# Performance work log

Measured on AMD Instinct MI355X. Metric: run time of the kernel, lower is better.

## Reference

```python
import jax, jax.numpy as jnp
import numpy as np

D_MODEL = 1024
NUM_HEADS = 16
D_K = D_MODEL // NUM_HEADS
B, T = 2, 2048


def setup_inputs() -> dict:
    key = jax.random.key(0)
    ks = jax.random.split(key, 9)
    s = 1.0 / np.sqrt(D_MODEL)
    inp = {"x": jax.random.normal(ks[0], (B, T, D_MODEL), dtype=jnp.float32)}
    for i, name in enumerate(["q", "k", "v", "out"]):
        inp[f"W_{name}"] = jax.random.uniform(ks[1 + 2 * i], (D_MODEL, D_MODEL), jnp.float32, -s, s)
        inp[f"b_{name}"] = jax.random.uniform(ks[2 + 2 * i], (D_MODEL,), jnp.float32, -s, s)
    return inp


def reference(x, W_q, b_q, W_k, b_k, W_v, b_v, W_out, b_out):
    b, t, _ = x.shape
    # torch Linear: y = x @ W.T + b
    def proj(inp, W, bias):
        y = inp @ W.T + bias
        return y.reshape(b, -1, NUM_HEADS, D_K).transpose(0, 2, 1, 3)  # [B,H,T,d_k]

    Q = proj(x, W_q, b_q)
    K = proj(x, W_k, b_k)
    V = proj(x, W_v, b_v)
    scores = jnp.einsum("bhqd,bhkd->bhqk", Q, K) / jnp.sqrt(jnp.float32(D_K))
    attn = jax.nn.softmax(scores, axis=-1)
    ctx = jnp.einsum("bhqk,bhkd->bhqd", attn, V)
    ctx = ctx.transpose(0, 2, 1, 3).reshape(b, t, D_MODEL)
    return ctx @ W_out.T + b_out
```

## Files before the change

### kernel.cpp

```cpp
#include <hip/hip_runtime.h>
#include <hip/hip_bf16.h>

typedef __attribute__((ext_vector_type(8))) short short8;
typedef __attribute__((ext_vector_type(4))) short short4v;
typedef __attribute__((ext_vector_type(4))) float floatx4;

__device__ __forceinline__ unsigned short f2b(float f) {
  unsigned int v;
  __builtin_memcpy(&v, &f, 4);
  unsigned int r = (v + 0x7FFFu + ((v >> 16) & 1u)) >> 16;
  return (unsigned short)r;
}

__device__ __forceinline__ unsigned int f2b_pk(float a, float b) {
  unsigned int ua, ub;
  __builtin_memcpy(&ua, &a, 4);
  __builtin_memcpy(&ub, &b, 4);
  ua = ua + 0x7FFFu + ((ua >> 16) & 1u);
  ub = ub + 0x7FFFu + ((ub >> 16) & 1u);
#if __has_builtin(__builtin_amdgcn_perm)
  return __builtin_amdgcn_perm(ub, ua, 0x07060302u);
#else
  return (ub & 0xFFFF0000u) | (ua >> 16);
#endif
}

__device__ __forceinline__ float fast_exp2(float x) {
#if __has_builtin(__builtin_amdgcn_exp2f)
  return __builtin_amdgcn_exp2f(x);
#else
  return __builtin_exp2f(x);
#endif
}

__device__ __forceinline__ void async_copy16(const void* g, void* l) {
  __builtin_amdgcn_global_load_lds(
      (const __attribute__((address_space(1))) unsigned int*)g,
      (__attribute__((address_space(3))) unsigned int*)l, 16, 0, 0);
}

#define QSCALE 0.18033688011112042f

__global__ __launch_bounds__(256) void cvt_all_kernel(
    const float* __restrict__ x,
    const float* __restrict__ w0, const float* __restrict__ w1,
    const float* __restrict__ w2, const float* __restrict__ w3,
    unsigned short* __restrict__ xb,
    unsigned short* __restrict__ d0, unsigned short* __restrict__ d1,
    unsigned short* __restrict__ d2, unsigned short* __restrict__ d3)
{
  int gid = blockIdx.x * 256 + threadIdx.x;
  const float* src;
  unsigned short* dst;
  size_t off;
  if (gid < (1 << 20)) {
    src = x; dst = xb; off = gid;
  } else {
    int g = gid - (1 << 20);
    int w = g >> 18;
    off = g & 0x3FFFF;
    src = (w == 0) ? w0 : (w == 1) ? w1 : (w == 2) ? w2 : w3;
    dst = (w == 0) ? d0 : (w == 1) ? d1 : (w == 2) ? d2 : d3;
  }
  floatx4 v = *(const floatx4*)(src + off * 4);
  unsigned int lo = f2b_pk(v[0], v[1]), hi = f2b_pk(v[2], v[3]);
  unsigned long long r = ((unsigned long long)hi << 32) | lo;
  *(unsigned long long*)(dst + off * 4) = r;
}

__global__ __launch_bounds__(256) void gemm_qkv_kernel(
    const unsigned short* __restrict__ A,
    const unsigned short* __restrict__ W0, const unsigned short* __restrict__ W1,
    const unsigned short* __restrict__ W2,
    const float* __restrict__ bias0, const float* __restrict__ bias1,
    const float* __restrict__ bias2,
    unsigned short* __restrict__ Qo, unsigned short* __restrict__ Ko,
    unsigned short* __restrict__ VTo)
{
  const int z = blockIdx.z;
  const unsigned short* W  = (z == 0) ? W0 : (z == 1) ? W1 : W2;
  const float* bias        = (z == 0) ? bias0 : (z == 1) ? bias1 : bias2;

  __shared__ alignas(16) unsigned short sA[128 * 32];
  __shared__ alignas(16) unsigned short sB[128 * 32];

  const int tid  = threadIdx.x;
  const int lane = tid & 63;
  const int wave = tid >> 6;
  const int col  = lane & 15;
  const int quad = lane >> 4;
  const int wm   = (wave >> 1) * 64;
  const int wn   = (wave & 1) * 64;
  const int m0   = blockIdx.y * 128;
  const int n0   = blockIdx.x * 128;
  const int swz8 = (quad ^ ((col >> 1) & 3)) * 8;

  floatx4 acc[4][4];
#pragma unroll
  for (int i = 0; i < 4; ++i)
#pragma unroll
    for (int j = 0; j < 4; ++j) acc[i][j] = (floatx4){0.f, 0.f, 0.f, 0.f};

  for (int k0 = 0; k0 < 1024; k0 += 32) {
    __syncthreads();
#pragma unroll
    for (int i = 0; i < 2; ++i) {
      int c   = i * 256 + tid;
      int row = c >> 2;
      int cs  = (c & 3) ^ ((c >> 3) & 3);
      int ko  = cs * 8;
      async_copy16(A + (size_t)(m0 + row) * 1024 + k0 + ko, sA + c * 8);
      async_copy16(W + (size_t)(n0 + row) * 1024 + k0 + ko, sB + c * 8);
    }
    __syncthreads();
    short8 af[4], bf[4];
#pragma unroll
    for (int mi = 0; mi < 4; ++mi)
      af[mi] = *(const short8*)(sA + (wm + mi * 16 + col) * 32 + swz8);
#pragma unroll
    for (int ni = 0; ni < 4; ++ni)
      bf[ni] = *(const short8*)(sB + (wn + ni * 16 + col) * 32 + swz8);
#pragma unroll
    for (int mi = 0; mi < 4; ++mi)
#pragma unroll
      for (int ni = 0; ni < 4; ++ni)
        acc[mi][ni] = __builtin_amdgcn_mfma_f32_16x16x32_bf16(af[mi], bf[ni], acc[mi][ni], 0, 0, 0);
  }

#pragma unroll
  for (int ni = 0; ni < 4; ++ni) {
    int n = n0 + wn + ni * 16 + col;
    float bv = bias[n];
#pragma unroll
    for (int mi = 0; mi < 4; ++mi) {
      int mbase = m0 + wm + mi * 16 + quad * 4;
      if (z == 2) {
        int d = n & 63, h = n >> 6;
        int bb = mbase >> 11, t = mbase & 2047;
        unsigned int lo = f2b_pk(acc[mi][ni][0] + bv, acc[mi][ni][1] + bv);
        unsigned int hi = f2b_pk(acc[mi][ni][2] + bv, acc[mi][ni][3] + bv);
        unsigned long long wv = ((unsigned long long)hi << 32) | lo;
        *(unsigned long long*)(VTo + (((size_t)bb * 16 + h) * 64 + d) * 2048 + t) = wv;
      } else {
#pragma unroll
        for (int r = 0; r < 4; ++r) {
          int m = mbase + r;
          float val = acc[mi][ni][r] + bv;
          if (z == 0) Qo[(size_t)m * 1024 + n] = f2b(val * QSCALE);
          else        Ko[(size_t)m * 1024 + n] = f2b(val);
        }
      }
    }
  }
}

__global__ __launch_bounds__(256) void gemm_out_kernel(
    const unsigned short* __restrict__ A, const unsigned short* __restrict__ W,
    const float* __restrict__ bias, float* __restrict__ DF)
{
  __shared__ alignas(16) unsigned short sA[128 * 32];
  __shared__ alignas(16) unsigned short sB[64 * 32];

  const int tid  = threadIdx.x;
  const int lane = tid & 63;
  const int wave = tid >> 6;
  const int col  = lane & 15;
  const int quad = lane >> 4;
  const int wm   = (wave >> 1) * 64;
  const int wn   = (wave & 1) * 32;
  const int m0   = blockIdx.y * 128;
  const int n0   = blockIdx.x * 64;
  const int swz8 = (quad ^ ((col >> 1) & 3)) * 8;

  floatx4 acc[4][2];
#pragma unroll
  for (int i = 0; i < 4; ++i)
#pragma unroll
    for (int j = 0; j < 2; ++j) acc[i][j] = (floatx4){0.f, 0.f, 0.f, 0.f};

  for (int k0 = 0; k0 < 1024; k0 += 32) {
    __syncthreads();
#pragma unroll
    for (int i = 0; i < 2; ++i) {
      int c   = i * 256 + tid;
      int row = c >> 2;
      int cs  = (c & 3) ^ ((c >> 3) & 3);
      async_copy16(A + (size_t)(m0 + row) * 1024 + k0 + cs * 8, sA + c * 8);
    }
    {
      int row = tid >> 2;
      int cs  = (tid & 3) ^ ((tid >> 3) & 3);
      async_copy16(W + (size_t)(n0 + row) * 1024 + k0 + cs * 8, sB + tid * 8);
    }
    __syncthreads();
    short8 af[4], bf[2];
#pragma unroll
    for (int mi = 0; mi < 4; ++mi)
      af[mi] = *(const short8*)(sA + (wm + mi * 16 + col) * 32 + swz8);
#pragma unroll
    for (int ni = 0; ni < 2; ++ni)
      bf[ni] = *(const short8*)(sB + (wn + ni * 16 + col) * 32 + swz8);
#pragma unroll
    for (int mi = 0; mi < 4; ++mi)
#pragma unroll
      for (int ni = 0; ni < 2; ++ni)
        acc[mi][ni] = __builtin_amdgcn_mfma_f32_16x16x32_bf16(af[mi], bf[ni], acc[mi][ni], 0, 0, 0);
  }

#pragma unroll
  for (int ni = 0; ni < 2; ++ni) {
    int n = n0 + wn + ni * 16 + col;
    float bv = bias[n];
#pragma unroll
    for (int mi = 0; mi < 4; ++mi) {
      int mbase = m0 + wm + mi * 16 + quad * 4;
#pragma unroll
      for (int r = 0; r < 4; ++r)
        DF[(size_t)(mbase + r) * 1024 + n] = acc[mi][ni][r] + bv;
    }
  }
}

__global__ __launch_bounds__(256, 2) void attention_kernel(
    const unsigned short* __restrict__ Q, const unsigned short* __restrict__ K,
    const unsigned short* __restrict__ VT, unsigned short* __restrict__ CTX)
{
  __shared__ alignas(16) unsigned short sK[2][4096];
  __shared__ alignas(16) unsigned short sV[2][4096];
  __shared__ alignas(16) unsigned short sP[4][32 * 64];

  const int flat = blockIdx.x;
  const int idx  = flat >> 3;
  const int bh   = (flat & 7) * 4 + (idx >> 4);
  const int q0   = (idx & 15) * 128;
  const int b = bh >> 4, h = bh & 15;

  const int tid  = threadIdx.x;
  const int lane = tid & 63;
  const int wave = tid >> 6;
  const int col  = lane & 15;
  const int quad = lane >> 4;
  const int c7   = col & 7;
  const int swz8 = (quad ^ ((col >> 1) & 3)) * 8;

  const int srow = tid >> 2;
  const int sko  = ((tid & 3) ^ ((tid >> 3) & 3)) * 8;

  const unsigned short* kbase = K + ((size_t)b * 2048 + srow) * 1024 + h * 64;
  const unsigned short* vbase = VT + ((size_t)bh * 64 + srow) * 2048;

  short8 qfA[2], qfB[2];
  {
    const unsigned short* qp =
        Q + ((size_t)(b * 2048 + q0 + wave * 32 + col)) * 1024 + h * 64 + quad * 8;
    qfA[0] = *(const short8*)qp;
    qfA[1] = *(const short8*)(qp + 32);
    qfB[0] = *(const short8*)(qp + 16 * 1024);
    qfB[1] = *(const short8*)(qp + 16 * 1024 + 32);
  }

#pragma unroll
  for (int i = 0; i < 2; ++i) {
    async_copy16(kbase + i * 32 + sko, sK[0] + (i * 256 + tid) * 8);
    async_copy16(vbase + i * 32 + sko, sV[0] + (i * 256 + tid) * 8);
  }

  floatx4 OA[4], OB[4];
#pragma unroll
  for (int f = 0; f < 4; ++f) {
    OA[f] = (floatx4){0.f, 0.f, 0.f, 0.f};
    OB[f] = (floatx4){0.f, 0.f, 0.f, 0.f};
  }
  float laccA = 0.f, laccB = 0.f;

  unsigned short* myP = &sP[wave][0];

#pragma unroll 2
  for (int kt = 0; kt < 2048; kt += 64) {
    const int cur = (kt >> 6) & 1;
    const unsigned short* sKc = sK[cur];
    const unsigned short* sVc = sV[cur];
    __syncthreads();
    if (kt + 64 < 2048) {
      const int nxt = cur ^ 1;
#pragma unroll
      for (int i = 0; i < 2; ++i) {
        async_copy16(kbase + (size_t)(kt + 64) * 1024 + i * 32 + sko,
                     sK[nxt] + (i * 256 + tid) * 8);
        async_copy16(vbase + (kt + 64) + i * 32 + sko,
                     sV[nxt] + (i * 256 + tid) * 8);
      }
    }

    floatx4 STA[4], STB[4];
    __builtin_amdgcn_s_setprio(1);
#pragma unroll
    for (int f = 0; f < 4; ++f) {
      short8 kf0 = *(const short8*)(sKc + (f * 16 + col) * 32 + swz8);
      short8 kf1 = *(const short8*)(sKc + 2048 + (f * 16 + col) * 32 + swz8);
      STA[f] = (floatx4){0.f, 0.f, 0.f, 0.f};
      STA[f] = __builtin_amdgcn_mfma_f32_16x16x32_bf16(kf0, qfA[0], STA[f], 0, 0, 0);
      STA[f] = __builtin_amdgcn_mfma_f32_16x16x32_bf16(kf1, qfA[1], STA[f], 0, 0, 0);
      STB[f] = (floatx4){0.f, 0.f, 0.f, 0.f};
      STB[f] = __builtin_amdgcn_mfma_f32_16x16x32_bf16(kf0, qfB[0], STB[f], 0, 0, 0);
      STB[f] = __builtin_amdgcn_mfma_f32_16x16x32_bf16(kf1, qfB[1], STB[f], 0, 0, 0);
    }
    __builtin_amdgcn_s_setprio(0);

#pragma unroll
    for (int f = 0; f < 4; ++f) {
      float a0 = fast_exp2(STA[f][0]);
      float a1 = fast_exp2(STA[f][1]);
      float a2 = fast_exp2(STA[f][2]);
      float a3 = fast_exp2(STA[f][3]);
      laccA += (a0 + a1) + (a2 + a3);
      unsigned long long wA =
          ((unsigned long long)f2b_pk(a2, a3) << 32) | f2b_pk(a0, a1);
      *(unsigned long long*)(myP + col * 64 +
                             (((f * 2 + (quad >> 1)) ^ c7) * 8) + (quad & 1) * 4) = wA;
      float b0 = fast_exp2(STB[f][0]);
      float b1 = fast_exp2(STB[f][1]);
      float b2 = fast_exp2(STB[f][2]);
      float b3 = fast_exp2(STB[f][3]);
      laccB += (b0 + b1) + (b2 + b3);
      unsigned long long wB =
          ((unsigned long long)f2b_pk(b2, b3) << 32) | f2b_pk(b0, b1);
      *(unsigned long long*)(myP + (16 + col) * 64 +
                             (((f * 2 + (quad >> 1)) ^ c7) * 8) + (quad & 1) * 4) = wB;
    }

    short8 pfA0 = *(const short8*)(myP + col * 64 + ((quad ^ c7) * 8));
    short8 pfA1 = *(const short8*)(myP + col * 64 + (((quad + 4) ^ c7) * 8));
    short8 pfB0 = *(const short8*)(myP + (16 + col) * 64 + ((quad ^ c7) * 8));
    short8 pfB1 = *(const short8*)(myP + (16 + col) * 64 + (((quad + 4) ^ c7) * 8));
    __builtin_amdgcn_s_setprio(1);
#pragma unroll
    for (int f = 0; f < 4; ++f) {
      short8 vf0 = *(const short8*)(sVc + (f * 16 + col) * 32 + swz8);
      short8 vf1 = *(const short8*)(sVc + 2048 + (f * 16 + col) * 32 + swz8);
      OA[f] = __builtin_amdgcn_mfma_f32_16x16x32_bf16(pfA0, vf0, OA[f], 0, 0, 0);
      OA[f] = __builtin_amdgcn_mfma_f32_16x16x32_bf16(pfA1, vf1, OA[f], 0, 0, 0);
      OB[f] = __builtin_amdgcn_mfma_f32_16x16x32_bf16(pfB0, vf0, OB[f], 0, 0, 0);
      OB[f] = __builtin_amdgcn_mfma_f32_16x16x32_bf16(pfB1, vf1, OB[f], 0, 0, 0);
    }
    __builtin_amdgcn_s_setprio(0);
  }

  laccA += __shfl_xor(laccA, 16, 64);
  laccA += __shfl_xor(laccA, 32, 64);
  laccB += __shfl_xor(laccB, 16, 64);
  laccB += __shfl_xor(laccB, 32, 64);
  float invA[4], invB[4];
#pragma unroll
  for (int r = 0; r < 4; ++r) {
    invA[r] = 1.f / __shfl(laccA, quad * 4 + r, 16);
    invB[r] = 1.f / __shfl(laccB, quad * 4 + r, 16);
  }

#pragma unroll
  for (int f = 0; f < 4; ++f) {
#pragma unroll
    for (int r = 0; r < 4; ++r) {
      int qA = q0 + wave * 32 + quad * 4 + r;
      int d = f * 16 + col;
      CTX[(size_t)(b * 2048 + qA) * 1024 + h * 64 + d] = f2b(OA[f][r] * invA[r]);
      CTX[(size_t)(b * 2048 + qA + 16) * 1024 + h * 64 + d] = f2b(OB[f][r] * invB[r]);
    }
  }
}

extern "C" void kernel_launch(void* const* d_in, const int* in_sizes, int n_in,
                              void* d_out, int out_size, void* d_ws, size_t ws_size,
                              hipStream_t stream) {
  const float* x   = (const float*)d_in[0];
  const float* W_q = (const float*)d_in[1];
  const float* b_q = (const float*)d_in[2];
  const float* W_k = (const float*)d_in[3];
  const float* b_k = (const float*)d_in[4];
  const float* W_v = (const float*)d_in[5];
  const float* b_v = (const float*)d_in[6];
  const float* W_o = (const float*)d_in[7];
  const float* b_o = (const float*)d_in[8];
  float* out = (float*)d_out;

  const size_t NX = (size_t)4096 * 1024;
  const size_t NW = (size_t)1024 * 1024;

  unsigned short* p   = (unsigned short*)d_ws;
  unsigned short* xb  = p;  p += NX;
  unsigned short* Wqb = p;  p += NW;
  unsigned short* Wkb = p;  p += NW;
  unsigned short* Wvb = p;  p += NW;
  unsigned short* Wob = p;  p += NW;
  unsigned short* Q   = p;  p += NX;
  unsigned short* Kb  = p;  p += NX;
  unsigned short* VT  = p;  p += NX;
  unsigned short* CTX = p;  p += NX;

  dim3 blk(256);
  cvt_all_kernel<<<dim3(8192), blk, 0, stream>>>(
      x, W_q, W_k, W_v, W_o, xb, Wqb, Wkb, Wvb, Wob);
  gemm_qkv_kernel<<<dim3(8, 32, 3), blk, 0, stream>>>(
      xb, Wqb, Wkb, Wvb, b_q, b_k, b_v, Q, Kb, VT);
  attention_kernel<<<dim3(512), blk, 0, stream>>>(Q, Kb, VT, CTX);
  gemm_out_kernel<<<dim3(16, 32), blk, 0, stream>>>(CTX, Wob, b_o, out);
}
```

Measured before the change: 190.8 us.

## Double-buffer GEMM shared tiles and halve attention block size

Both projection GEMMs now prefetch the next K-slice into a second shared-memory buffer while computing on the current one. This removes one barrier per iteration and hides global-load latency. The attention kernel switches to 128-thread blocks covering 64 query rows each, launches twice as many blocks, and gives each thread four K/V staging copies per stage. This raises the block count and allows finer scheduling across CUs, at the cost of less K/V reuse per block and doubled LDS per GEMM block.

Result: slower. 202.6 us (+6.2%).

```diff
diff --git a/kernel.cpp b/kernel.cpp
--- a/kernel.cpp
+++ b/kernel.cpp
@@ -81,8 +81,8 @@
   const unsigned short* W  = (z == 0) ? W0 : (z == 1) ? W1 : W2;
   const float* bias        = (z == 0) ? bias0 : (z == 1) ? bias1 : bias2;
 
-  __shared__ alignas(16) unsigned short sA[128 * 32];
-  __shared__ alignas(16) unsigned short sB[128 * 32];
+  __shared__ alignas(16) unsigned short sA[2][128 * 32];
+  __shared__ alignas(16) unsigned short sB[2][128 * 32];
 
   const int tid  = threadIdx.x;
   const int lane = tid & 63;
@@ -95,31 +95,38 @@
   const int n0   = blockIdx.x * 128;
   const int swz8 = (quad ^ ((col >> 1) & 3)) * 8;
 
+  const int scs = ((tid & 3) ^ ((tid >> 3) & 3)) * 8;
+  const unsigned short* Abase = A + (size_t)(m0 + (tid >> 2)) * 1024 + scs;
+  const unsigned short* Wbase = W + (size_t)(n0 + (tid >> 2)) * 1024 + scs;
+
   floatx4 acc[4][4];
 #pragma unroll
   for (int i = 0; i < 4; ++i)
 #pragma unroll
     for (int j = 0; j < 4; ++j) acc[i][j] = (floatx4){0.f, 0.f, 0.f, 0.f};
 
+  async_copy16(Abase, sA[0] + tid * 8);
+  async_copy16(Abase + 65536, sA[0] + (256 + tid) * 8);
+  async_copy16(Wbase, sB[0] + tid * 8);
+  async_copy16(Wbase + 65536, sB[0] + (256 + tid) * 8);
+
   for (int k0 = 0; k0 < 1024; k0 += 32) {
+    const int cur = (k0 >> 5) & 1;
     __syncthreads();
-#pragma unroll
-    for (int i = 0; i < 2; ++i) {
-      int c   = i * 256 + tid;
-      int row = c >> 2;
-      int cs  = (c & 3) ^ ((c >> 3) & 3);
-      int ko  = cs * 8;
-      async_copy16(A + (size_t)(m0 + row) * 1024 + k0 + ko, sA + c * 8);
-      async_copy16(W + (size_t)(n0 + row) * 1024 + k0 + ko, sB + c * 8);
-    }
-    __syncthreads();
+    if (k0 + 32 < 1024) {
+      const int nxt = cur ^ 1;
+      async_copy16(Abase + k0 + 32, sA[nxt] + tid * 8);
+      async_copy16(Abase + 65536 + k0 + 32, sA[nxt] + (256 + tid) * 8);
+      async_copy16(Wbase + k0 + 32, sB[nxt] + tid * 8);
+      async_copy16(Wbase + 65536 + k0 + 32, sB[nxt] + (256 + tid) * 8);
+    }
     short8 af[4], bf[4];
 #pragma unroll
     for (int mi = 0; mi < 4; ++mi)
-      af[mi] = *(const short8*)(sA + (wm + mi * 16 + col) * 32 + swz8);
+      af[mi] = *(const short8*)(sA[cur] + (wm + mi * 16 + col) * 32 + swz8);
 #pragma unroll
     for (int ni = 0; ni < 4; ++ni)
-      bf[ni] = *(const short8*)(sB + (wn + ni * 16 + col) * 32 + swz8);
+      bf[ni] = *(const short8*)(sB[cur] + (wn + ni * 16 + col) * 32 + swz8);
 #pragma unroll
     for (int mi = 0; mi < 4; ++mi)
 #pragma unroll
@@ -158,8 +165,8 @@
     const unsigned short* __restrict__ A, const unsigned short* __restrict__ W,
     const float* __restrict__ bias, float* __restrict__ DF)
 {
-  __shared__ alignas(16) unsigned short sA[128 * 32];
-  __shared__ alignas(16) unsigned short sB[64 * 32];
+  __shared__ alignas(16) unsigned short sA[2][128 * 32];
+  __shared__ alignas(16) unsigned short sB[2][64 * 32];
 
   const int tid  = threadIdx.x;
   const int lane = tid & 63;
@@ -172,34 +179,36 @@
   const int n0   = blockIdx.x * 64;
   const int swz8 = (quad ^ ((col >> 1) & 3)) * 8;
 
+  const int scs = ((tid & 3) ^ ((tid >> 3) & 3)) * 8;
+  const unsigned short* Abase = A + (size_t)(m0 + (tid >> 2)) * 1024 + scs;
+  const unsigned short* Wbase = W + (size_t)(n0 + (tid >> 2)) * 1024 + scs;
+
   floatx4 acc[4][2];
 #pragma unroll
   for (int i = 0; i < 4; ++i)
 #pragma unroll
     for (int j = 0; j < 2; ++j) acc[i][j] = (floatx4){0.f, 0.f, 0.f, 0.f};
 
+  async_copy16(Abase, sA[0] + tid * 8);
+  async_copy16(Abase + 65536, sA[0] + (256 + tid) * 8);
+  async_copy16(Wbase, sB[0] + tid * 8);
+
   for (int k0 = 0; k0 < 1024; k0 += 32) {
+    const int cur = (k0 >> 5) & 1;
     __syncthreads();
-#pragma unroll
-    for (int i = 0; i < 2; ++i) {
-      int c   = i * 256 + tid;
-      int row = c >> 2;
-      int cs  = (c & 3) ^ ((c >> 3) & 3);
-      async_copy16(A + (size_t)(m0 + row) * 1024 + k0 + cs * 8, sA + c * 8);
-    }
-    {
-      int row = tid >> 2;
-      int cs  = (tid & 3) ^ ((tid >> 3) & 3);
-      async_copy16(W + (size_t)(n0 + row) * 1024 + k0 + cs * 8, sB + tid * 8);
-    }
-    __syncthreads();
+    if (k0 + 32 < 1024) {
+      const int nxt = cur ^ 1;
+      async_copy16(Abase + k0 + 32, sA[nxt] + tid * 8);
+      async_copy16(Abase + 65536 + k0 + 32, sA[nxt] + (256 + tid) * 8);
+      async_copy16(Wbase + k0 + 32, sB[nxt] + tid * 8);
+    }
     short8 af[4], bf[2];
 #pragma unroll
     for (int mi = 0; mi < 4; ++mi)
-      af[mi] = *(const short8*)(sA + (wm + mi * 16 + col) * 32 + swz8);
+      af[mi] = *(const short8*)(sA[cur] + (wm + mi * 16 + col) * 32 + swz8);
 #pragma unroll
     for (int ni = 0; ni < 2; ++ni)
-      bf[ni] = *(const short8*)(sB + (wn + ni * 16 + col) * 32 + swz8);
+      bf[ni] = *(const short8*)(sB[cur] + (wn + ni * 16 + col) * 32 + swz8);
 #pragma unroll
     for (int mi = 0; mi < 4; ++mi)
 #pragma unroll
@@ -221,18 +230,18 @@
   }
 }
 
-__global__ __launch_bounds__(256, 2) void attention_kernel(
+__global__ __launch_bounds__(128, 2) void attention_kernel(
     const unsigned short* __restrict__ Q, const unsigned short* __restrict__ K,
     const unsigned short* __restrict__ VT, unsigned short* __restrict__ CTX)
 {
   __shared__ alignas(16) unsigned short sK[2][4096];
   __shared__ alignas(16) unsigned short sV[2][4096];
-  __shared__ alignas(16) unsigned short sP[4][32 * 64];
+  __shared__ alignas(16) unsigned short sP[2][32 * 64];
 
   const int flat = blockIdx.x;
   const int idx  = flat >> 3;
-  const int bh   = (flat & 7) * 4 + (idx >> 4);
-  const int q0   = (idx & 15) * 128;
+  const int bh   = (flat & 7) * 4 + (idx >> 5);
+  const int q0   = (idx & 31) * 64;
   const int b = bh >> 4, h = bh & 15;
 
   const int tid  = threadIdx.x;
@@ -259,11 +268,21 @@
     qfB[1] = *(const short8*)(qp + 16 * 1024 + 32);
   }
 
-#pragma unroll
-  for (int i = 0; i < 2; ++i) {
-    async_copy16(kbase + i * 32 + sko, sK[0] + (i * 256 + tid) * 8);
-    async_copy16(vbase + i * 32 + sko, sV[0] + (i * 256 + tid) * 8);
-  }
+#define STAGE_KV(ktv, buf)                                                     \
+  do {                                                                         \
+    const unsigned short* kp = kbase + (size_t)(ktv) * 1024 + sko;             \
+    async_copy16(kp, sK[buf] + tid * 8);                                       \
+    async_copy16(kp + 32 * 1024, sK[buf] + (128 + tid) * 8);                   \
+    async_copy16(kp + 32, sK[buf] + (256 + tid) * 8);                          \
+    async_copy16(kp + 32 * 1024 + 32, sK[buf] + (384 + tid) * 8);              \
+    const unsigned short* vp = vbase + (ktv) + sko;                            \
+    async_copy16(vp, sV[buf] + tid * 8);                                       \
+    async_copy16(vp + 32 * 2048, sV[buf] + (128 + tid) * 8);                   \
+    async_copy16(vp + 32, sV[buf] + (256 + tid) * 8);                          \
+    async_copy16(vp + 32 * 2048 + 32, sV[buf] + (384 + tid) * 8);              \
+  } while (0)
+
+  STAGE_KV(0, 0);
 
   floatx4 OA[4], OB[4];
 #pragma unroll
@@ -282,14 +301,7 @@
     const unsigned short* sVc = sV[cur];
     __syncthreads();
     if (kt + 64 < 2048) {
-      const int nxt = cur ^ 1;
-#pragma unroll
-      for (int i = 0; i < 2; ++i) {
-        async_copy16(kbase + (size_t)(kt + 64) * 1024 + i * 32 + sko,
-                     sK[nxt] + (i * 256 + tid) * 8);
-        async_copy16(vbase + (kt + 64) + i * 32 + sko,
-                     sV[nxt] + (i * 256 + tid) * 8);
-      }
+      STAGE_KV(kt + 64, cur ^ 1);
     }
 
     floatx4 STA[4], STB[4];
@@ -397,11 +409,10 @@
   unsigned short* VT  = p;  p += NX;
   unsigned short* CTX = p;  p += NX;
 
-  dim3 blk(256);
-  cvt_all_kernel<<<dim3(8192), blk, 0, stream>>>(
+  cvt_all_kernel<<<dim3(8192), dim3(256), 0, stream>>>(
       x, W_q, W_k, W_v, W_o, xb, Wqb, Wkb, Wvb, Wob);
-  gemm_qkv_kernel<<<dim3(8, 32, 3), blk, 0, stream>>>(
+  gemm_qkv_kernel<<<dim3(8, 32, 3), dim3(256), 0, stream>>>(
       xb, Wqb, Wkb, Wvb, b_q, b_k, b_v, Q, Kb, VT);
-  attention_kernel<<<dim3(512), blk, 0, stream>>>(Q, Kb, VT, CTX);
-  gemm_out_kernel<<<dim3(16, 32), blk, 0, stream>>>(CTX, Wob, b_o, out);
-}
+  attention_kernel<<<dim3(1024), dim3(128), 0, stream>>>(Q, Kb, VT, CTX);
+  gemm_out_kernel<<<dim3(16, 32), dim3(256), 0, stream>>>(CTX, Wob, b_o, out);
+}
```
